# Kernel tuning notes

Hardware: AMD Instinct MI355X
Metric: run time of the kernel (lower is better)

The kernel has to match this reference:

```python
import jax, jax.numpy as jnp
import numpy as np

# pool sizes (must match init_kwargs)
N_FQK, N_FV, N_REL, N_VAL, N_KNOW = 512, 256, 128, 32, 256
K_FQK, K_FV, K_REL, K_VAL = 64, 32, 16, 3
D_MODEL, D_SPACE = 1024, 64
B, S = 8, 2048


def _topk_sparsify(w, k):
    # keep top-k entries per row, zero the rest (values unchanged)
    vals, idx = jax.lax.top_k(w, k)                      # [B,k]
    out = jnp.zeros_like(w)
    rows = jnp.arange(w.shape[0])[:, None]
    return out.at[rows, idx].set(vals), idx


def setup_inputs() -> dict:
    key = jax.random.key(0)
    k1, k2, k3, k4 = jax.random.split(key, 4)
    x = jax.random.normal(k1, (B, S, D_MODEL), dtype=jnp.float32)
    # importance: per-token weights normalized over sequence
    importance = jax.nn.softmax(jax.random.normal(k2, (B, S), dtype=jnp.float32), axis=-1)
    W = jax.random.normal(k3, (D_MODEL, D_SPACE), dtype=jnp.float32) * 0.02
    b = jnp.zeros((D_SPACE,), dtype=jnp.float32)
    total = N_FQK + N_FV + N_REL + N_VAL + N_KNOW
    neuron_emb = jax.random.normal(k4, (total, D_SPACE), dtype=jnp.float32) * 0.02
    return {"x": x, "importance": importance, "W": W, "b": b, "neuron_emb": neuron_emb}


def reference(x, importance, W, b, neuron_emb):
    # projection (dropout inactive in eval); normalized neuron embeddings
    h = x @ W + b                                         # [B,S,d_space]
    emb_n = neuron_emb / jnp.linalg.norm(neuron_emb, axis=-1, keepdims=True)
    all_logits = jnp.einsum('bsd,nd->bsn', h, emb_n)      # [B,S,N_total]

    e0 = N_FQK
    e1 = e0 + N_FV
    e2 = e1 + N_REL
    e3 = e2 + N_VAL

    def route(lo, hi):
        pref = jax.nn.softmax(all_logits[..., lo:hi], axis=-1)  # [B,S,n]
        w = jnp.einsum('bs,bsn->bn', importance, pref)          # [B,n]
        return pref, w

    _, w_qk = route(0, e0)
    _, idx_qk = jax.lax.top_k(w_qk, K_FQK)
    idx_qk = jnp.sort(idx_qk, axis=-1)

    _, w_v = route(e0, e1)
    _, idx_v = jax.lax.top_k(w_v, K_FV)
    idx_v = jnp.sort(idx_v, axis=-1)

    # relational Q and K share the same logit slice (eval: no excitability bonus)
    _, w_rQ = route(e1, e2)
    _, w_rK = route(e1, e2)
    rw_Q, _ = _topk_sparsify(w_rQ, K_REL)
    rw_K, _ = _topk_sparsify(w_rK, K_REL)

    _, w_val = route(e2, e3)
    vw, _ = _topk_sparsify(w_val, K_VAL)

    return idx_qk, idx_v, rw_Q, rw_K, vw, w_qk, w_v
```

## Files before the change

### kernel.cpp

```cpp
#include <hip/hip_runtime.h>
#include <hip/hip_bf16.h>
#include <hip/hip_fp16.h>
#include <math.h>

#define ROWS  16384
#define DM    1024
#define DS    64
#define NUSE  928
#define NPAD  960
#define NT    15

typedef __attribute__((ext_vector_type(8))) short bf16x8;
typedef __attribute__((ext_vector_type(4))) float f32x4;

static __device__ inline f32x4 mfma16(bf16x8 a, bf16x8 b, f32x4 c) {
    return __builtin_amdgcn_mfma_f32_16x16x32_bf16(a, b, c, 0, 0, 0);
}

static __device__ inline void bfsplit(float v, unsigned short& h, unsigned short& l) {
    unsigned u = __float_as_uint(v);
    unsigned hr = u + 0x7FFFu + ((u >> 16) & 1u);
    h = (unsigned short)(hr >> 16);
    float hf = __uint_as_float((unsigned)h << 16);
    float r = v - hf;
    unsigned ur = __float_as_uint(r);
    unsigned lr2 = ur + 0x7FFFu + ((ur >> 16) & 1u);
    l = (unsigned short)(lr2 >> 16);
}

#define OFF_EBH  0LL
#define OFF_EBL  122880LL
#define OFF_WBH  245760LL
#define OFF_WBL  376832LL
#define OFF_WP   507904LL

__global__ __launch_bounds__(256) void k_prep(const float* __restrict__ emb,
                                              const float* __restrict__ W,
                                              unsigned short* __restrict__ ebh,
                                              unsigned short* __restrict__ ebl,
                                              unsigned short* __restrict__ wbh,
                                              unsigned short* __restrict__ wbl) {
    if (blockIdx.x < 4) {
        int n = blockIdx.x * 256 + threadIdx.x;
        if (n >= NPAD) return;
        if (n >= NUSE) {
            #pragma unroll
            for (int d = 0; d < DS; d++) {
                int kt = d >> 5, q = (d >> 3) & 3, j = d & 7;
                int a = ((kt * 4 + q) * NPAD + n) * 8 + j;
                ebh[a] = 0; ebl[a] = 0;
            }
            return;
        }
        float ss = 0.f;
        #pragma unroll
        for (int d = 0; d < DS; d++) { float v = emb[n * DS + d]; ss = fmaf(v, v, ss); }
        float inv = 1.0f / sqrtf(ss);
        #pragma unroll
        for (int d = 0; d < DS; d++) {
            float v = emb[n * DS + d] * inv;
            unsigned short h, l; bfsplit(v, h, l);
            int kt = d >> 5, q = (d >> 3) & 3, j = d & 7;
            int a = ((kt * 4 + q) * NPAD + n) * 8 + j;
            ebh[a] = h; ebl[a] = l;
        }
    } else {
        int idx = (blockIdx.x - 4) * 256 + threadIdx.x;
        int ktg = idx >> 6, n = idx & 63;
        #pragma unroll
        for (int q = 0; q < 4; q++) {
            #pragma unroll
            for (int j = 0; j < 8; j++) {
                int k = ktg * 32 + q * 8 + j;
                float v = W[k * DS + n];
                unsigned short h, l; bfsplit(v, h, l);
                int a = ((ktg * 4 + q) * 64 + n) * 8 + j;
                wbh[a] = h; wbl[a] = l;
            }
        }
    }
}

__global__ __launch_bounds__(512, 4) void k_mega(const float* __restrict__ x,
                                                 const float* __restrict__ bias,
                                                 const unsigned short* __restrict__ wbh,
                                                 const unsigned short* __restrict__ wbl,
                                                 const unsigned short* __restrict__ ebh,
                                                 const unsigned short* __restrict__ ebl,
                                                 const float* __restrict__ imp,
                                                 float* __restrict__ wpart) {
    __shared__ __align__(16) unsigned char smem[79872];
    unsigned short* Ph = (unsigned short*)smem;
    float* Cbuf = (float*)smem;
    unsigned short* Hh = (unsigned short*)(smem + 69120);
    unsigned short* Hl = (unsigned short*)(smem + 73216);
    float* zslot = (float*)(smem + 77312);
    float* coefL = (float*)(smem + 79360);

    const int tid = threadIdx.x;
    const int rc = blockIdx.x;
    const long long row0 = (long long)rc * 32;
    const int w = tid >> 6, lane = tid & 63, q = lane >> 4, lm = lane & 15;

    zslot[tid] = 0.f;

    const int rg = w >> 2, kg = w & 3;
    {
        const float* xp = &x[(row0 + rg * 16 + lm) * (long long)DM + kg * 256 + q * 8];
        f32x4 acc[4];
        #pragma unroll
        for (int f = 0; f < 4; f++) { acc[f].x = 0.f; acc[f].y = 0.f; acc[f].z = 0.f; acc[f].w = 0.f; }

        #pragma unroll
        for (int ks = 0; ks < 8; ks++) {
            float4 v0 = *(const float4*)&xp[ks * 32];
            float4 v1 = *(const float4*)&xp[ks * 32 + 4];
            union { bf16x8 v; unsigned short s[8]; } ah, al;
            bfsplit(v0.x, ah.s[0], al.s[0]); bfsplit(v0.y, ah.s[1], al.s[1]);
            bfsplit(v0.z, ah.s[2], al.s[2]); bfsplit(v0.w, ah.s[3], al.s[3]);
            bfsplit(v1.x, ah.s[4], al.s[4]); bfsplit(v1.y, ah.s[5], al.s[5]);
            bfsplit(v1.z, ah.s[6], al.s[6]); bfsplit(v1.w, ah.s[7], al.s[7]);
            const int ktg = kg * 8 + ks;
            #pragma unroll
            for (int f = 0; f < 4; f++) {
                const int ba = ((ktg * 4 + q) * 64 + f * 16 + lm) * 8;
                const bf16x8 b_h = *(const bf16x8*)&wbh[ba];
                const bf16x8 b_l = *(const bf16x8*)&wbl[ba];
                acc[f] = mfma16(ah.v, b_h, acc[f]);
                acc[f] = mfma16(ah.v, b_l, acc[f]);
                acc[f] = mfma16(al.v, b_h, acc[f]);
            }
        }
        #pragma unroll
        for (int f = 0; f < 4; f++)
            #pragma unroll
            for (int t = 0; t < 4; t++)
                Cbuf[w * 1088 + (q * 4 + t) * 68 + f * 16 + lm] = acc[f][t];
    }
    __syncthreads();

    {
        const int r = tid >> 4, seg = tid & 15;
        const int rgg = r >> 4, rl = r & 15;
        const int c0 = seg * 4;
        float4 s = *(const float4*)&bias[c0];
        #pragma unroll
        for (int g = 0; g < 4; g++) {
            float4 a = *(const float4*)&Cbuf[(rgg * 4 + g) * 1088 + rl * 68 + c0];
            s.x += a.x; s.y += a.y; s.z += a.z; s.w += a.w;
        }
        __syncthreads();
        unsigned short h0, l0, h1, l1, h2, l2, h3, l3;
        bfsplit(s.x, h0, l0); bfsplit(s.y, h1, l1);
        bfsplit(s.z, h2, l2); bfsplit(s.w, h3, l3);
        const int ktH = c0 >> 5, qH = (c0 >> 3) & 3, jH = c0 & 7;
        const int base = ((ktH * 4 + qH) * 32 + r) * 8 + jH;
        uint2 ph; ph.x = (unsigned)h0 | ((unsigned)h1 << 16); ph.y = (unsigned)h2 | ((unsigned)h3 << 16);
        uint2 pl; pl.x = (unsigned)l0 | ((unsigned)l1 << 16); pl.y = (unsigned)l2 | ((unsigned)l3 << 16);
        *(uint2*)&Hh[base] = ph;
        *(uint2*)&Hl[base] = pl;
    }
    __syncthreads();

    const int wg = w & 3, rgp = w >> 2;
    bf16x8 a_h[2], a_l[2];
    #pragma unroll
    for (int kt = 0; kt < 2; kt++) {
        const int ab = ((kt * 4 + q) * 32 + rgp * 16 + lm) * 8;
        a_h[kt] = *(const bf16x8*)&Hh[ab];
        a_l[kt] = *(const bf16x8*)&Hl[ab];
    }

    #pragma unroll
    for (int v = 0; v < 4; v++) {
        const int nt = wg + v * 4;
        if (nt > 14) continue;
        f32x4 acc[4];
        #pragma unroll
        for (int f = 0; f < 4; f++) { acc[f].x = 0.f; acc[f].y = 0.f; acc[f].z = 0.f; acc[f].w = 0.f; }
        #pragma unroll
        for (int kt = 0; kt < 2; kt++) {
            #pragma unroll
            for (int f = 0; f < 4; f++) {
                const int bb = ((kt * 4 + q) * NPAD + nt * 64 + f * 16 + lm) * 8;
                const bf16x8 b_h = *(const bf16x8*)&ebh[bb];
                const bf16x8 b_l = *(const bf16x8*)&ebl[bb];
                acc[f] = mfma16(a_h[kt], b_h, acc[f]);
                acc[f] = mfma16(a_h[kt], b_l, acc[f]);
                acc[f] = mfma16(a_l[kt], b_h, acc[f]);
            }
        }
        const int sl = (nt < 8) ? 0 : (nt < 12) ? 1 : (nt < 14) ? 2 : 3;
        float s0 = 0.f, s1 = 0.f, s2 = 0.f, s3 = 0.f;
        #pragma unroll
        for (int f = 0; f < 4; f++) {
            float e0 = __expf(acc[f][0]);
            float e1 = __expf(acc[f][1]);
            float e2 = __expf(acc[f][2]);
            float e3 = __expf(acc[f][3]);
            const int n = nt * 64 + f * 16 + lm;
            unsigned short p0 = __half_as_ushort(__float2half(e0));
            unsigned short p1 = __half_as_ushort(__float2half(e1));
            unsigned short p2 = __half_as_ushort(__float2half(e2));
            unsigned short p3 = __half_as_ushort(__float2half(e3));
            uint2 pk; pk.x = (unsigned)p0 | ((unsigned)p1 << 16); pk.y = (unsigned)p2 | ((unsigned)p3 << 16);
            *(uint2*)&Ph[n * 36 + rgp * 16 + q * 4] = pk;
            if (nt * 64 + f * 16 < NUSE) {
                s0 += e0; s1 += e1; s2 += e2; s3 += e3;
            }
        }
        #pragma unroll
        for (int off = 1; off < 16; off <<= 1) {
            s0 += __shfl_xor(s0, off); s1 += __shfl_xor(s1, off);
            s2 += __shfl_xor(s2, off); s3 += __shfl_xor(s3, off);
        }
        if (lm < 4) {
            float sv = (lm == 0) ? s0 : (lm == 1) ? s1 : (lm == 2) ? s2 : s3;
            zslot[(wg * 4 + sl) * 32 + rgp * 16 + q * 4 + lm] += sv;
        }
    }
    __syncthreads();

    if (tid < 32) {
        const int r = tid;
        const float im = imp[row0 + r];
        #pragma unroll
        for (int sl = 0; sl < 4; sl++) {
            float Z = zslot[(0 * 4 + sl) * 32 + r] + zslot[(1 * 4 + sl) * 32 + r]
                    + zslot[(2 * 4 + sl) * 32 + r] + zslot[(3 * 4 + sl) * 32 + r];
            coefL[r * 4 + sl] = im / Z;
        }
    }
    __syncthreads();

    for (int nn = tid; nn < NUSE; nn += 512) {
        const int sl = (nn < 512) ? 0 : (nn < 768) ? 1 : (nn < 896) ? 2 : 3;
        float acc = 0.f;
        #pragma unroll
        for (int rb = 0; rb < 8; rb++) {
            uint2 pk = *(const uint2*)&Ph[nn * 36 + rb * 4];
            float v0 = __half2float(__ushort_as_half((unsigned short)(pk.x & 0xFFFF)));
            float v1 = __half2float(__ushort_as_half((unsigned short)(pk.x >> 16)));
            float v2 = __half2float(__ushort_as_half((unsigned short)(pk.y & 0xFFFF)));
            float v3 = __half2float(__ushort_as_half((unsigned short)(pk.y >> 16)));
            const int row = rb * 4;
            acc = fmaf(coefL[(row + 0) * 4 + sl], v0, acc);
            acc = fmaf(coefL[(row + 1) * 4 + sl], v1, acc);
            acc = fmaf(coefL[(row + 2) * 4 + sl], v2, acc);
            acc = fmaf(coefL[(row + 3) * 4 + sl], v3, acc);
        }
        wpart[(long long)rc * NPAD + nn] = acc;
    }
}

__global__ __launch_bounds__(512) void k_out(const float* __restrict__ wpart,
                                             float* __restrict__ out) {
    const int b = blockIdx.x;
    const int tid = threadIdx.x;
    __shared__ float w_s[NUSE];
    __shared__ int   rk[NUSE];

    for (int n = tid; n < NUSE; n += 512) {
        float s = 0.f;
        #pragma unroll 4
        for (int c = 0; c < 64; c++)
            s += wpart[(long long)(b * 64 + c) * NPAD + n];
        w_s[n] = s;
        if (n < 512)      out[3072 + (long long)b * 512 + n] = s;
        else if (n < 768) out[7168 + (long long)b * 256 + (n - 512)] = s;
    }
    __syncthreads();

    for (int n = tid; n < NUSE; n += 512) {
        int lo, hi;
        if (n < 512)      { lo = 0;   hi = 512; }
        else if (n < 768) { lo = 512; hi = 768; }
        else if (n < 896) { lo = 768; hi = 896; }
        else              { lo = 896; hi = NUSE; }
        float wn = w_s[n];
        int r = 0;
        for (int m = lo; m < hi; m++) {
            float wm = w_s[m];
            r += (wm > wn) || ((wm == wn) && (m < n));
        }
        rk[n] = r;
    }
    __syncthreads();

    if (tid < 512) {
        int n = tid;
        if (rk[n] < 64) {
            int pos = 0;
            for (int m = 0; m < n; m++) pos += (rk[m] < 64) ? 1 : 0;
            out[(long long)b * 64 + pos] = (float)n;
        }
    }
    if (tid < 256) {
        int n = 512 + tid;
        if (rk[n] < 32) {
            int pos = 0;
            for (int m = 512; m < n; m++) pos += (rk[m] < 32) ? 1 : 0;
            out[512 + (long long)b * 32 + pos] = (float)tid;
        }
    }
    if (tid < 128) {
        int n = 768 + tid;
        float v = (rk[n] < 16) ? w_s[n] : 0.f;
        out[768 + (long long)b * 128 + tid] = v;
        out[1792 + (long long)b * 128 + tid] = v;
    }
    if (tid < 32) {
        int n = 896 + tid;
        float v = (rk[n] < 3) ? w_s[n] : 0.f;
        out[2816 + (long long)b * 32 + tid] = v;
    }
}

extern "C" void kernel_launch(void* const* d_in, const int* in_sizes, int n_in,
                              void* d_out, int out_size, void* d_ws, size_t ws_size,
                              hipStream_t stream) {
    const float* x    = (const float*)d_in[0];
    const float* imp  = (const float*)d_in[1];
    const float* W    = (const float*)d_in[2];
    const float* bias = (const float*)d_in[3];
    const float* emb  = (const float*)d_in[4];

    char* ws = (char*)d_ws;
    unsigned short* ebh = (unsigned short*)(ws + OFF_EBH);
    unsigned short* ebl = (unsigned short*)(ws + OFF_EBL);
    unsigned short* wbh = (unsigned short*)(ws + OFF_WBH);
    unsigned short* wbl = (unsigned short*)(ws + OFF_WBL);
    float* wpart        = (float*)(ws + OFF_WP);
    float* out          = (float*)d_out;

    k_prep<<<12, 256, 0, stream>>>(emb, W, ebh, ebl, wbh, wbl);
    k_mega<<<512, 512, 0, stream>>>(x, bias, wbh, wbl, ebh, ebl, imp, wpart);
    k_out<<<8, 512, 0, stream>>>(wpart, out);
}
```

Before: 169.5 us.

## Halve rows per block to 16 and split K across all eight waves

Each block of the fused projection+routing kernel now handles 16 rows instead of 32, with all 8 waves splitting the 1024-wide K dimension for the x@W stage and then each taking up to two neuron tiles. Shared memory drops to about 40KB and the launch bound asks for 8 blocks/CU, aiming for more resident blocks to hide latency on the memory-bound x stream. In exchange, the 8-way partial-sum reduction adds LDS traffic, the embedding tiles are reloaded by twice as many blocks, and k_out must reduce 128 partials per batch instead of 64.

```diff
diff --git a/kernel.cpp b/kernel.cpp
--- a/kernel.cpp
+++ b/kernel.cpp
@@ -8,7 +8,8 @@
 #define DS    64
 #define NUSE  928
 #define NPAD  960
-#define NT    15
+#define RPB   16
+#define NBLK  (ROWS/RPB)
 
 typedef __attribute__((ext_vector_type(8))) short bf16x8;
 typedef __attribute__((ext_vector_type(4))) float f32x4;
@@ -81,7 +82,7 @@
     }
 }
 
-__global__ __launch_bounds__(512, 4) void k_mega(const float* __restrict__ x,
+__global__ __launch_bounds__(512, 8) void k_mega(const float* __restrict__ x,
                                                  const float* __restrict__ bias,
                                                  const unsigned short* __restrict__ wbh,
                                                  const unsigned short* __restrict__ wbl,
@@ -89,30 +90,30 @@
                                                  const unsigned short* __restrict__ ebl,
                                                  const float* __restrict__ imp,
                                                  float* __restrict__ wpart) {
-    __shared__ __align__(16) unsigned char smem[79872];
-    unsigned short* Ph = (unsigned short*)smem;
-    float* Cbuf = (float*)smem;
-    unsigned short* Hh = (unsigned short*)(smem + 69120);
-    unsigned short* Hl = (unsigned short*)(smem + 73216);
-    float* zslot = (float*)(smem + 77312);
-    float* coefL = (float*)(smem + 79360);
+    __shared__ __align__(16) unsigned char smem[40960];
+    unsigned short* Ph   = (unsigned short*)smem;
+    float*          Cb   = (float*)smem;
+    unsigned short* Hh   = (unsigned short*)(smem + 34560);
+    unsigned short* Hl   = (unsigned short*)(smem + 36608);
+    float*          zslot = (float*)(smem + 38656);
+    float*          coefL = (float*)(smem + 40704);
 
     const int tid = threadIdx.x;
     const int rc = blockIdx.x;
-    const long long row0 = (long long)rc * 32;
+    const long long row0 = (long long)rc * RPB;
     const int w = tid >> 6, lane = tid & 63, q = lane >> 4, lm = lane & 15;
 
     zslot[tid] = 0.f;
 
-    const int rg = w >> 2, kg = w & 3;
     {
-        const float* xp = &x[(row0 + rg * 16 + lm) * (long long)DM + kg * 256 + q * 8];
+        const int kg = w;
+        const float* xp = &x[(row0 + lm) * (long long)DM + kg * 128 + q * 8];
         f32x4 acc[4];
         #pragma unroll
         for (int f = 0; f < 4; f++) { acc[f].x = 0.f; acc[f].y = 0.f; acc[f].z = 0.f; acc[f].w = 0.f; }
 
         #pragma unroll
-        for (int ks = 0; ks < 8; ks++) {
+        for (int ks = 0; ks < 4; ks++) {
             float4 v0 = *(const float4*)&xp[ks * 32];
             float4 v1 = *(const float4*)&xp[ks * 32 + 4];
             union { bf16x8 v; unsigned short s[8]; } ah, al;
@@ -120,7 +121,7 @@
             bfsplit(v0.z, ah.s[2], al.s[2]); bfsplit(v0.w, ah.s[3], al.s[3]);
             bfsplit(v1.x, ah.s[4], al.s[4]); bfsplit(v1.y, ah.s[5], al.s[5]);
             bfsplit(v1.z, ah.s[6], al.s[6]); bfsplit(v1.w, ah.s[7], al.s[7]);
-            const int ktg = kg * 8 + ks;
+            const int ktg = kg * 4 + ks;
             #pragma unroll
             for (int f = 0; f < 4; f++) {
                 const int ba = ((ktg * 4 + q) * 64 + f * 16 + lm) * 8;
@@ -133,47 +134,38 @@
         }
         #pragma unroll
         for (int f = 0; f < 4; f++)
-            #pragma unroll
-            for (int t = 0; t < 4; t++)
-                Cbuf[w * 1088 + (q * 4 + t) * 68 + f * 16 + lm] = acc[f][t];
-    }
-    __syncthreads();
-
-    {
-        const int r = tid >> 4, seg = tid & 15;
-        const int rgg = r >> 4, rl = r & 15;
-        const int c0 = seg * 4;
-        float4 s = *(const float4*)&bias[c0];
-        #pragma unroll
-        for (int g = 0; g < 4; g++) {
-            float4 a = *(const float4*)&Cbuf[(rgg * 4 + g) * 1088 + rl * 68 + c0];
-            s.x += a.x; s.y += a.y; s.z += a.z; s.w += a.w;
-        }
-        __syncthreads();
-        unsigned short h0, l0, h1, l1, h2, l2, h3, l3;
-        bfsplit(s.x, h0, l0); bfsplit(s.y, h1, l1);
-        bfsplit(s.z, h2, l2); bfsplit(s.w, h3, l3);
-        const int ktH = c0 >> 5, qH = (c0 >> 3) & 3, jH = c0 & 7;
-        const int base = ((ktH * 4 + qH) * 32 + r) * 8 + jH;
-        uint2 ph; ph.x = (unsigned)h0 | ((unsigned)h1 << 16); ph.y = (unsigned)h2 | ((unsigned)h3 << 16);
-        uint2 pl; pl.x = (unsigned)l0 | ((unsigned)l1 << 16); pl.y = (unsigned)l2 | ((unsigned)l3 << 16);
-        *(uint2*)&Hh[base] = ph;
-        *(uint2*)&Hl[base] = pl;
-    }
-    __syncthreads();
-
-    const int wg = w & 3, rgp = w >> 2;
+            *(f32x4*)&Cb[(w * 64 + lane) * 16 + f * 4] = acc[f];
+    }
+    __syncthreads();
+
+    #pragma unroll
+    for (int ee = 0; ee < 2; ee++) {
+        const int e = tid * 2 + ee;
+        float s = 0.f;
+        #pragma unroll
+        for (int g = 0; g < 8; g++) s += Cb[g * 1024 + e];
+        const int L = e >> 4, r = e & 15, f = r >> 2, t = r & 3;
+        const int row = (L >> 4) * 4 + t;
+        const int col = f * 16 + (L & 15);
+        s += bias[col];
+        unsigned short hh, ll; bfsplit(s, hh, ll);
+        const int kt = col >> 5, qH = (col >> 3) & 3, j = col & 7;
+        const int hidx = ((kt * 4 + qH) * RPB + row) * 8 + j;
+        Hh[hidx] = hh; Hl[hidx] = ll;
+    }
+    __syncthreads();
+
     bf16x8 a_h[2], a_l[2];
     #pragma unroll
     for (int kt = 0; kt < 2; kt++) {
-        const int ab = ((kt * 4 + q) * 32 + rgp * 16 + lm) * 8;
+        const int ab = ((kt * 4 + q) * RPB + lm) * 8;
         a_h[kt] = *(const bf16x8*)&Hh[ab];
         a_l[kt] = *(const bf16x8*)&Hl[ab];
     }
 
     #pragma unroll
-    for (int v = 0; v < 4; v++) {
-        const int nt = wg + v * 4;
+    for (int v = 0; v < 2; v++) {
+        const int nt = w + v * 8;
         if (nt > 14) continue;
         f32x4 acc[4];
         #pragma unroll
@@ -203,8 +195,8 @@
             unsigned short p1 = __half_as_ushort(__float2half(e1));
             unsigned short p2 = __half_as_ushort(__float2half(e2));
             unsigned short p3 = __half_as_ushort(__float2half(e3));
-            uint2 pk; pk.x = (unsigned)p0 | ((unsigned)p1 << 16); pk.y = (unsigned)p2 | ((unsigned)p3 << 16);
-            *(uint2*)&Ph[n * 36 + rgp * 16 + q * 4] = pk;
+            *(unsigned*)&Ph[n * 18 + q * 4]     = (unsigned)p0 | ((unsigned)p1 << 16);
+            *(unsigned*)&Ph[n * 18 + q * 4 + 2] = (unsigned)p2 | ((unsigned)p3 << 16);
             if (nt * 64 + f * 16 < NUSE) {
                 s0 += e0; s1 += e1; s2 += e2; s3 += e3;
             }
@@ -216,18 +208,19 @@
         }
         if (lm < 4) {
             float sv = (lm == 0) ? s0 : (lm == 1) ? s1 : (lm == 2) ? s2 : s3;
-            zslot[(wg * 4 + sl) * 32 + rgp * 16 + q * 4 + lm] += sv;
-        }
-    }
-    __syncthreads();
-
-    if (tid < 32) {
+            zslot[(w * 4 + sl) * RPB + q * 4 + lm] += sv;
+        }
+    }
+    __syncthreads();
+
+    if (tid < RPB) {
         const int r = tid;
         const float im = imp[row0 + r];
         #pragma unroll
         for (int sl = 0; sl < 4; sl++) {
-            float Z = zslot[(0 * 4 + sl) * 32 + r] + zslot[(1 * 4 + sl) * 32 + r]
-                    + zslot[(2 * 4 + sl) * 32 + r] + zslot[(3 * 4 + sl) * 32 + r];
+            float Z = 0.f;
+            #pragma unroll
+            for (int g = 0; g < 8; g++) Z += zslot[(g * 4 + sl) * RPB + r];
             coefL[r * 4 + sl] = im / Z;
         }
     }
@@ -238,16 +231,11 @@
         float acc = 0.f;
         #pragma unroll
         for (int rb = 0; rb < 8; rb++) {
-            uint2 pk = *(const uint2*)&Ph[nn * 36 + rb * 4];
-            float v0 = __half2float(__ushort_as_half((unsigned short)(pk.x & 0xFFFF)));
-            float v1 = __half2float(__ushort_as_half((unsigned short)(pk.x >> 16)));
-            float v2 = __half2float(__ushort_as_half((unsigned short)(pk.y & 0xFFFF)));
-            float v3 = __half2float(__ushort_as_half((unsigned short)(pk.y >> 16)));
-            const int row = rb * 4;
-            acc = fmaf(coefL[(row + 0) * 4 + sl], v0, acc);
-            acc = fmaf(coefL[(row + 1) * 4 + sl], v1, acc);
-            acc = fmaf(coefL[(row + 2) * 4 + sl], v2, acc);
-            acc = fmaf(coefL[(row + 3) * 4 + sl], v3, acc);
+            const unsigned pk = *(const unsigned*)&Ph[nn * 18 + rb * 2];
+            float v0 = __half2float(__ushort_as_half((unsigned short)(pk & 0xFFFF)));
+            float v1 = __half2float(__ushort_as_half((unsigned short)(pk >> 16)));
+            acc = fmaf(coefL[(rb * 2 + 0) * 4 + sl], v0, acc);
+            acc = fmaf(coefL[(rb * 2 + 1) * 4 + sl], v1, acc);
         }
         wpart[(long long)rc * NPAD + nn] = acc;
     }
@@ -263,8 +251,8 @@
     for (int n = tid; n < NUSE; n += 512) {
         float s = 0.f;
         #pragma unroll 4
-        for (int c = 0; c < 64; c++)
-            s += wpart[(long long)(b * 64 + c) * NPAD + n];
+        for (int c = 0; c < 128; c++)
+            s += wpart[(long long)(b * 128 + c) * NPAD + n];
         w_s[n] = s;
         if (n < 512)      out[3072 + (long long)b * 512 + n] = s;
         else if (n < 768) out[7168 + (long long)b * 256 + (n - 512)] = s;
@@ -334,6 +322,6 @@
     float* out          = (float*)d_out;
 
     k_prep<<<12, 256, 0, stream>>>(emb, W, ebh, ebl, wbh, wbl);
-    k_mega<<<512, 512, 0, stream>>>(x, bias, wbh, wbl, ebh, ebl, imp, wpart);
+    k_mega<<<NBLK, 512, 0, stream>>>(x, bias, wbh, wbl, ebh, ebl, imp, wpart);
     k_out<<<8, 512, 0, stream>>>(wpart, out);
 }
```

Result: slower. 183.5 us (+8.2%).

## Stage x through double-buffered LDS and parallelize partial-sum reduction

Applied to the files above, without the earlier changes.

The projection GEMM now loads x in row-major chunks with coalesced float4 reads, converts each chunk to hi/lo bf16 once, and writes it to a double-buffered LDS tile. The next chunk's global load is issued while the current chunk's MFMAs run. Separately, the serial 64-way reduction of per-block partial weights in the 8-block output kernel moves into a new k_red kernel spread over 232 blocks, and the ranking kernel now just reads the reduced values. This adds a kernel launch and one barrier per chunk in exchange for better load coalescing, overlap, and parallelism in the reduction.

```diff
diff --git a/kernel.cpp b/kernel.cpp
--- a/kernel.cpp
+++ b/kernel.cpp
@@ -8,7 +8,8 @@
 #define DS    64
 #define NUSE  928
 #define NPAD  960
-#define NT    15
+#define RPB   32
+#define NBLK  (ROWS/RPB)
 
 typedef __attribute__((ext_vector_type(8))) short bf16x8;
 typedef __attribute__((ext_vector_type(4))) float f32x4;
@@ -33,6 +34,7 @@
 #define OFF_WBH  245760LL
 #define OFF_WBL  376832LL
 #define OFF_WP   507904LL
+#define OFF_WR   2473984LL
 
 __global__ __launch_bounds__(256) void k_prep(const float* __restrict__ emb,
                                               const float* __restrict__ W,
@@ -90,53 +92,81 @@
                                                  const float* __restrict__ imp,
                                                  float* __restrict__ wpart) {
     __shared__ __align__(16) unsigned char smem[79872];
-    unsigned short* Ph = (unsigned short*)smem;
-    float* Cbuf = (float*)smem;
-    unsigned short* Hh = (unsigned short*)(smem + 69120);
-    unsigned short* Hl = (unsigned short*)(smem + 73216);
-    float* zslot = (float*)(smem + 77312);
-    float* coefL = (float*)(smem + 79360);
+    unsigned short* Ph    = (unsigned short*)smem;
+    float*          Cb    = (float*)smem;
+    unsigned short* Hh    = (unsigned short*)(smem + 69120);
+    unsigned short* Hl    = (unsigned short*)(smem + 73216);
+    float*          zslot = (float*)(smem + 77312);
+    float*          coefL = (float*)(smem + 79360);
 
     const int tid = threadIdx.x;
     const int rc = blockIdx.x;
-    const long long row0 = (long long)rc * 32;
+    const long long row0 = (long long)rc * RPB;
     const int w = tid >> 6, lane = tid & 63, q = lane >> 4, lm = lane & 15;
 
     zslot[tid] = 0.f;
 
     const int rg = w >> 2, kg = w & 3;
+    const int srow = tid >> 4, sjg = tid & 15;
+    const int skt = sjg >> 2, sq = sjg & 3;
+    const int sidx = ((skt * 4 + sq) * 32 + srow) * 8;
+    const float* xp = &x[(row0 + srow) * (long long)DM + sjg * 8];
+
+    f32x4 acc[4];
+    #pragma unroll
+    for (int f = 0; f < 4; f++) { acc[f].x = 0.f; acc[f].y = 0.f; acc[f].z = 0.f; acc[f].w = 0.f; }
+
+    float4 pv0 = *(const float4*)&xp[0];
+    float4 pv1 = *(const float4*)&xp[4];
     {
-        const float* xp = &x[(row0 + rg * 16 + lm) * (long long)DM + kg * 256 + q * 8];
-        f32x4 acc[4];
-        #pragma unroll
-        for (int f = 0; f < 4; f++) { acc[f].x = 0.f; acc[f].y = 0.f; acc[f].z = 0.f; acc[f].w = 0.f; }
-
-        #pragma unroll
-        for (int ks = 0; ks < 8; ks++) {
-            float4 v0 = *(const float4*)&xp[ks * 32];
-            float4 v1 = *(const float4*)&xp[ks * 32 + 4];
-            union { bf16x8 v; unsigned short s[8]; } ah, al;
-            bfsplit(v0.x, ah.s[0], al.s[0]); bfsplit(v0.y, ah.s[1], al.s[1]);
-            bfsplit(v0.z, ah.s[2], al.s[2]); bfsplit(v0.w, ah.s[3], al.s[3]);
-            bfsplit(v1.x, ah.s[4], al.s[4]); bfsplit(v1.y, ah.s[5], al.s[5]);
-            bfsplit(v1.z, ah.s[6], al.s[6]); bfsplit(v1.w, ah.s[7], al.s[7]);
-            const int ktg = kg * 8 + ks;
+        union { uint4 u; unsigned short s[8]; } ah, al;
+        bfsplit(pv0.x, ah.s[0], al.s[0]); bfsplit(pv0.y, ah.s[1], al.s[1]);
+        bfsplit(pv0.z, ah.s[2], al.s[2]); bfsplit(pv0.w, ah.s[3], al.s[3]);
+        bfsplit(pv1.x, ah.s[4], al.s[4]); bfsplit(pv1.y, ah.s[5], al.s[5]);
+        bfsplit(pv1.z, ah.s[6], al.s[6]); bfsplit(pv1.w, ah.s[7], al.s[7]);
+        *(uint4*)&((unsigned short*)(smem))[sidx]         = ah.u;
+        *(uint4*)&((unsigned short*)(smem + 16384))[sidx] = al.u;
+    }
+
+    for (int ch = 0; ch < 8; ch++) {
+        if (ch < 7) {
+            pv0 = *(const float4*)&xp[(ch + 1) * 128];
+            pv1 = *(const float4*)&xp[(ch + 1) * 128 + 4];
+        }
+        __syncthreads();
+        {
+            const unsigned short* XhB = (const unsigned short*)(smem + (ch & 1) * 8192);
+            const unsigned short* XlB = (const unsigned short*)(smem + 16384 + (ch & 1) * 8192);
+            const bf16x8 a_h = *(const bf16x8*)&XhB[((kg * 4 + q) * 32 + rg * 16 + lm) * 8];
+            const bf16x8 a_l = *(const bf16x8*)&XlB[((kg * 4 + q) * 32 + rg * 16 + lm) * 8];
+            const int ktg = ch * 4 + kg;
             #pragma unroll
             for (int f = 0; f < 4; f++) {
                 const int ba = ((ktg * 4 + q) * 64 + f * 16 + lm) * 8;
                 const bf16x8 b_h = *(const bf16x8*)&wbh[ba];
                 const bf16x8 b_l = *(const bf16x8*)&wbl[ba];
-                acc[f] = mfma16(ah.v, b_h, acc[f]);
-                acc[f] = mfma16(ah.v, b_l, acc[f]);
-                acc[f] = mfma16(al.v, b_h, acc[f]);
-            }
-        }
-        #pragma unroll
-        for (int f = 0; f < 4; f++)
-            #pragma unroll
-            for (int t = 0; t < 4; t++)
-                Cbuf[w * 1088 + (q * 4 + t) * 68 + f * 16 + lm] = acc[f][t];
-    }
+                acc[f] = mfma16(a_h, b_h, acc[f]);
+                acc[f] = mfma16(a_h, b_l, acc[f]);
+                acc[f] = mfma16(a_l, b_h, acc[f]);
+            }
+        }
+        if (ch < 7) {
+            union { uint4 u; unsigned short s[8]; } ah, al;
+            bfsplit(pv0.x, ah.s[0], al.s[0]); bfsplit(pv0.y, ah.s[1], al.s[1]);
+            bfsplit(pv0.z, ah.s[2], al.s[2]); bfsplit(pv0.w, ah.s[3], al.s[3]);
+            bfsplit(pv1.x, ah.s[4], al.s[4]); bfsplit(pv1.y, ah.s[5], al.s[5]);
+            bfsplit(pv1.z, ah.s[6], al.s[6]); bfsplit(pv1.w, ah.s[7], al.s[7]);
+            *(uint4*)&((unsigned short*)(smem + ((ch + 1) & 1) * 8192))[sidx]         = ah.u;
+            *(uint4*)&((unsigned short*)(smem + 16384 + ((ch + 1) & 1) * 8192))[sidx] = al.u;
+        }
+    }
+    __syncthreads();
+
+    #pragma unroll
+    for (int f = 0; f < 4; f++)
+        #pragma unroll
+        for (int t = 0; t < 4; t++)
+            Cb[w * 1088 + (q * 4 + t) * 68 + f * 16 + lm] = acc[f][t];
     __syncthreads();
 
     {
@@ -146,7 +176,7 @@
         float4 s = *(const float4*)&bias[c0];
         #pragma unroll
         for (int g = 0; g < 4; g++) {
-            float4 a = *(const float4*)&Cbuf[(rgg * 4 + g) * 1088 + rl * 68 + c0];
+            float4 a = *(const float4*)&Cb[(rgg * 4 + g) * 1088 + rl * 68 + c0];
             s.x += a.x; s.y += a.y; s.z += a.z; s.w += a.w;
         }
         __syncthreads();
@@ -175,9 +205,9 @@
     for (int v = 0; v < 4; v++) {
         const int nt = wg + v * 4;
         if (nt > 14) continue;
-        f32x4 acc[4];
-        #pragma unroll
-        for (int f = 0; f < 4; f++) { acc[f].x = 0.f; acc[f].y = 0.f; acc[f].z = 0.f; acc[f].w = 0.f; }
+        f32x4 acc2[4];
+        #pragma unroll
+        for (int f = 0; f < 4; f++) { acc2[f].x = 0.f; acc2[f].y = 0.f; acc2[f].z = 0.f; acc2[f].w = 0.f; }
         #pragma unroll
         for (int kt = 0; kt < 2; kt++) {
             #pragma unroll
@@ -185,19 +215,19 @@
                 const int bb = ((kt * 4 + q) * NPAD + nt * 64 + f * 16 + lm) * 8;
                 const bf16x8 b_h = *(const bf16x8*)&ebh[bb];
                 const bf16x8 b_l = *(const bf16x8*)&ebl[bb];
-                acc[f] = mfma16(a_h[kt], b_h, acc[f]);
-                acc[f] = mfma16(a_h[kt], b_l, acc[f]);
-                acc[f] = mfma16(a_l[kt], b_h, acc[f]);
+                acc2[f] = mfma16(a_h[kt], b_h, acc2[f]);
+                acc2[f] = mfma16(a_h[kt], b_l, acc2[f]);
+                acc2[f] = mfma16(a_l[kt], b_h, acc2[f]);
             }
         }
         const int sl = (nt < 8) ? 0 : (nt < 12) ? 1 : (nt < 14) ? 2 : 3;
         float s0 = 0.f, s1 = 0.f, s2 = 0.f, s3 = 0.f;
         #pragma unroll
         for (int f = 0; f < 4; f++) {
-            float e0 = __expf(acc[f][0]);
-            float e1 = __expf(acc[f][1]);
-            float e2 = __expf(acc[f][2]);
-            float e3 = __expf(acc[f][3]);
+            float e0 = __expf(acc2[f][0]);
+            float e1 = __expf(acc2[f][1]);
+            float e2 = __expf(acc2[f][2]);
+            float e3 = __expf(acc2[f][3]);
             const int n = nt * 64 + f * 16 + lm;
             unsigned short p0 = __half_as_ushort(__float2half(e0));
             unsigned short p1 = __half_as_ushort(__float2half(e1));
@@ -235,7 +265,7 @@
 
     for (int nn = tid; nn < NUSE; nn += 512) {
         const int sl = (nn < 512) ? 0 : (nn < 768) ? 1 : (nn < 896) ? 2 : 3;
-        float acc = 0.f;
+        float accw = 0.f;
         #pragma unroll
         for (int rb = 0; rb < 8; rb++) {
             uint2 pk = *(const uint2*)&Ph[nn * 36 + rb * 4];
@@ -244,27 +274,46 @@
             float v2 = __half2float(__ushort_as_half((unsigned short)(pk.y & 0xFFFF)));
             float v3 = __half2float(__ushort_as_half((unsigned short)(pk.y >> 16)));
             const int row = rb * 4;
-            acc = fmaf(coefL[(row + 0) * 4 + sl], v0, acc);
-            acc = fmaf(coefL[(row + 1) * 4 + sl], v1, acc);
-            acc = fmaf(coefL[(row + 2) * 4 + sl], v2, acc);
-            acc = fmaf(coefL[(row + 3) * 4 + sl], v3, acc);
-        }
-        wpart[(long long)rc * NPAD + nn] = acc;
-    }
-}
-
-__global__ __launch_bounds__(512) void k_out(const float* __restrict__ wpart,
-                                             float* __restrict__ out) {
+            accw = fmaf(coefL[(row + 0) * 4 + sl], v0, accw);
+            accw = fmaf(coefL[(row + 1) * 4 + sl], v1, accw);
+            accw = fmaf(coefL[(row + 2) * 4 + sl], v2, accw);
+            accw = fmaf(coefL[(row + 3) * 4 + sl], v3, accw);
+        }
+        wpart[(long long)rc * NPAD + nn] = accw;
+    }
+}
+
+__global__ __launch_bounds__(256) void k_red(const float* __restrict__ wpart,
+                                             float* __restrict__ wred) {
+    const int g = blockIdx.x;
+    const int b = blockIdx.y;
+    const int tid = threadIdx.x;
+    const int n = g * 32 + (tid & 31);
+    const int cp = tid >> 5;
+    float s = 0.f;
+    #pragma unroll 2
+    for (int c = cp; c < 64; c += 8)
+        s += wpart[(long long)(b * 64 + c) * NPAD + n];
+    __shared__ float red[8][32];
+    red[cp][tid & 31] = s;
+    __syncthreads();
+    if (tid < 32) {
+        float t = 0.f;
+        #pragma unroll
+        for (int p = 0; p < 8; p++) t += red[p][tid];
+        wred[b * 960 + g * 32 + tid] = t;
+    }
+}
+
+__global__ __launch_bounds__(512) void k_rank(const float* __restrict__ wred,
+                                              float* __restrict__ out) {
     const int b = blockIdx.x;
     const int tid = threadIdx.x;
     __shared__ float w_s[NUSE];
     __shared__ int   rk[NUSE];
 
     for (int n = tid; n < NUSE; n += 512) {
-        float s = 0.f;
-        #pragma unroll 4
-        for (int c = 0; c < 64; c++)
-            s += wpart[(long long)(b * 64 + c) * NPAD + n];
+        float s = wred[b * 960 + n];
         w_s[n] = s;
         if (n < 512)      out[3072 + (long long)b * 512 + n] = s;
         else if (n < 768) out[7168 + (long long)b * 256 + (n - 512)] = s;
@@ -331,9 +380,11 @@
     unsigned short* wbh = (unsigned short*)(ws + OFF_WBH);
     unsigned short* wbl = (unsigned short*)(ws + OFF_WBL);
     float* wpart        = (float*)(ws + OFF_WP);
+    float* wred         = (float*)(ws + OFF_WR);
     float* out          = (float*)d_out;
 
     k_prep<<<12, 256, 0, stream>>>(emb, W, ebh, ebl, wbh, wbl);
-    k_mega<<<512, 512, 0, stream>>>(x, bias, wbh, wbl, ebh, ebl, imp, wpart);
-    k_out<<<8, 512, 0, stream>>>(wpart, out);
-}
+    k_mega<<<NBLK, 512, 0, stream>>>(x, bias, wbh, wbl, ebh, ebl, imp, wpart);
+    k_red<<<dim3(29, 8), 256, 0, stream>>>(wpart, wred);
+    k_rank<<<8, 512, 0, stream>>>(wred, out);
+}
```

New measurement: 158.6 us. 6.5% less time.
